# Performance work log

Hardware: AMD Instinct MI355X
Metric: run time of the kernel (lower is better)

Reference implementation:

```python
import jax, jax.numpy as jnp
import numpy as np

N_FFT = 1024
HOP = 512


def _overlap_add_50pct(frames):
    """Stateful 50% overlap-add. frames: (B, N, n_fft) -> (B, N, hop).
    Each frame is split into (curr, next); output[t] = curr[t] + next[t-1]."""
    xs = jnp.moveaxis(frames, 1, 0)  # (N, B, n_fft) for scan over frames

    def step(carry, x):
        x_curr = x[..., :HOP]
        x_next = x[..., HOP:]
        return x_next, x_curr + carry

    init = jnp.zeros((xs.shape[1], HOP), dtype=frames.dtype)
    _, ys = jax.lax.scan(step, init, xs)  # ys: (N, B, hop)
    return jnp.moveaxis(ys, 0, 1)  # (B, N, hop)


def _istft(re, im):
    spec = jax.lax.complex(re, im)               # (B, N, n_fft//2+1)
    frames = jnp.fft.irfft(spec, n=N_FFT, axis=-1)  # (B, N, n_fft), real IFFT
    frames = frames * jnp.asarray(0.5, frames.dtype)  # MulHalf (window_fn=None path)
    return _overlap_add_50pct(frames)            # (B, N, hop)


def setup_inputs() -> dict:
    key = jax.random.key(0)
    k1, k2 = jax.random.split(key)
    B, N = 8, 4000
    re = jax.random.normal(k1, (B, N, N_FFT // 2 + 1), dtype=jnp.float32)
    im = jax.random.normal(k2, (B, N, N_FFT // 2 + 1), dtype=jnp.float32)
    return {"re": re, "im": im}


def reference(re, im):
    return _istft(re, im)
```

## Files before the change

### kernel.cpp

```cpp
#include <hip/hip_runtime.h>
#include <math.h>

#define NBINS 513
#define NROWS 4000
#define BATCH 8
#define FPW   8
#define CHAINS_PER_BATCH (NROWS / FPW)

typedef const __attribute__((address_space(1))) void* gvp;
typedef __attribute__((address_space(3))) void* lvp;

__device__ __forceinline__ void cmul(float& ar, float& ai, float br, float bi) {
    const float t = ar * br - ai * bi;
    ai = ar * bi + ai * br;
    ar = t;
}

__device__ __forceinline__ void idft8(float* xr, float* xi) {
    const float S = 0.70710678118654752440f;
    float er[4], ei[4], orr[4], oi[4];
    #pragma unroll
    for (int j = 0; j < 4; ++j) {
        er[j]  = xr[j] + xr[j+4];  ei[j] = xi[j] + xi[j+4];
        orr[j] = xr[j] - xr[j+4];  oi[j] = xi[j] - xi[j+4];
    }
    const float f1r = S * (orr[1] - oi[1]), f1i = S * (orr[1] + oi[1]);
    const float f2r = -oi[2],               f2i = orr[2];
    const float f3r = S * (-orr[3] - oi[3]), f3i = S * (orr[3] - oi[3]);
    {
        const float eer = er[0]+er[2], eei = ei[0]+ei[2];
        const float eor = er[0]-er[2], eoi = ei[0]-ei[2];
        const float oer = er[1]+er[3], oei = ei[1]+ei[3];
        const float oor = er[1]-er[3], ooi = ei[1]-ei[3];
        xr[0] = eer + oer;  xi[0] = eei + oei;
        xr[2] = eor - ooi;  xi[2] = eoi + oor;
        xr[4] = eer - oer;  xi[4] = eei - oei;
        xr[6] = eor + ooi;  xi[6] = eoi - oor;
    }
    {
        const float eer = orr[0]+f2r, eei = oi[0]+f2i;
        const float eor = orr[0]-f2r, eoi = oi[0]-f2i;
        const float oer = f1r+f3r,    oei = f1i+f3i;
        const float oor = f1r-f3r,    ooi = f1i-f3i;
        xr[1] = eer + oer;  xi[1] = eei + oei;
        xr[3] = eor - ooi;  xi[3] = eoi + oor;
        xr[5] = eer - oer;  xi[5] = eei - oei;
        xr[7] = eor + ooi;  xi[7] = eoi - oor;
    }
}

__global__ __launch_bounds__(64) void istft_kernel(
    const float* __restrict__ re, const float* __restrict__ im,
    float* __restrict__ out)
{
    __shared__ float  st[2][2][516];
    __shared__ float2 ex2[512];

    const int u  = threadIdx.x;
    const int b  = blockIdx.y;
    const int t0 = blockIdx.x * FPW;

    const int k1 = u >> 3;
    const int k2 = u & 7;

    const float w0 = 6.283185307179586476925f / 1024.0f;
    const float F  = 4.8828125e-4f;

    float2 twn[8];
    #pragma unroll
    for (int j = 0; j < 8; ++j) {
        float s, c; sincosf(w0 * (float)(u + 64 * j), &s, &c);
        twn[j] = make_float2(-F * s, F * c);
    }
    float2 wA, wB0, wBs;
    {
        float s, c;
        sincosf(w0 * (float)(16 * k1), &s, &c);     wA  = make_float2(c, s);
        sincosf(w0 * (float)(2 * k2 * k1), &s, &c); wB0 = make_float2(c, s);
        sincosf(w0 * (float)(16 * k2), &s, &c);     wBs = make_float2(c, s);
    }

    float2 cc[4];
    #pragma unroll
    for (int m = 0; m < 4; ++m) cc[m] = make_float2(0.f, 0.f);

    const float* rebase = re + (size_t)b * NROWS * NBINS;
    const float* imbase = im + (size_t)b * NROWS * NBINS;

    auto stage = [&](int t, int buf) {
        const float* rp = rebase + (size_t)t * NBINS;
        const float* ip = imbase + (size_t)t * NBINS;
        #pragma unroll
        for (int jj = 0; jj < 8; ++jj)
            __builtin_amdgcn_global_load_lds((gvp)(rp + 64 * jj + u),
                                             (lvp)&st[buf][0][64 * jj], 4, 0, 0);
        __builtin_amdgcn_global_load_lds((gvp)(rp + 449 + u),
                                         (lvp)&st[buf][0][449], 4, 0, 0);
        #pragma unroll
        for (int jj = 0; jj < 8; ++jj)
            __builtin_amdgcn_global_load_lds((gvp)(ip + 64 * jj + u),
                                             (lvp)&st[buf][1][64 * jj], 4, 0, 0);
        __builtin_amdgcn_global_load_lds((gvp)(ip + 449 + u),
                                         (lvp)&st[buf][1][449], 4, 0, 0);
    };

    if (t0 == 0) {
        #pragma unroll
        for (int j = 0; j < 8; ++j) { st[0][0][u + 64 * j] = 0.f; st[0][1][u + 64 * j] = 0.f; }
        if (u == 0) { st[0][0][512] = 0.f; st[0][1][512] = 0.f; }
    } else {
        stage(t0 - 1, 0);
    }
    asm volatile("s_waitcnt vmcnt(0)" ::: "memory");

    for (int it = 0; it <= FPW; ++it) {
        const int t = t0 - 1 + it;
        const int c = it & 1;

        if (it >= 2)      { asm volatile("s_waitcnt vmcnt(8)" ::: "memory"); }
        else if (it == 1) { asm volatile("s_waitcnt vmcnt(0)" ::: "memory"); }

        float zr8[8], zi8[8];
        {
            const float* fr = st[c][0];
            const float* fi = st[c][1];
            #pragma unroll
            for (int j = 0; j < 8; ++j) {
                const int k = u + 64 * j;
                float xr = fr[k], xi = fi[k];
                float rc = fr[512 - k], ic = -fi[512 - k];
                if (k == 0) { xi = 0.f; ic = 0.f; }
                const float er0 = xr + rc, ei0 = xi + ic;
                const float hr0 = xr - rc, hi0 = xi - ic;
                zr8[j] = F * er0 + (twn[j].x * hr0 - twn[j].y * hi0);
                zi8[j] = F * ei0 + (twn[j].x * hi0 + twn[j].y * hr0);
            }
        }

        if (it < FPW) stage(t + 1, c ^ 1);

        idft8(zr8, zi8);
        {
            float tr = wA.x, ti = wA.y;
            #pragma unroll
            for (int m0 = 1; m0 < 8; ++m0) {
                cmul(zr8[m0], zi8[m0], tr, ti);
                cmul(tr, ti, wA.x, wA.y);
            }
        }
        #pragma unroll
        for (int m0 = 0; m0 < 8; ++m0)
            ex2[64 * m0 + 8 * ((k1 ^ m0) & 7) + k2] = make_float2(zr8[m0], zi8[m0]);
        #pragma unroll
        for (int kk = 0; kk < 8; ++kk) {
            const float2 v = ex2[64 * k1 + 8 * ((kk ^ k1) & 7) + k2];
            zr8[kk] = v.x; zi8[kk] = v.y;
        }

        idft8(zr8, zi8);
        {
            float tr = wB0.x, ti = wB0.y;
            #pragma unroll
            for (int m1 = 0; m1 < 8; ++m1) {
                cmul(zr8[m1], zi8[m1], tr, ti);
                cmul(tr, ti, wBs.x, wBs.y);
            }
        }
        #pragma unroll
        for (int m1 = 0; m1 < 8; ++m1)
            ex2[64 * k2 + 8 * ((m1 ^ k2) & 7) + k1] = make_float2(zr8[m1], zi8[m1]);
        #pragma unroll
        for (int kk = 0; kk < 8; ++kk) {
            const float2 v = ex2[64 * kk + 8 * ((k1 ^ kk) & 7) + k2];
            zr8[kk] = v.x; zi8[kk] = v.y;
        }

        idft8(zr8, zi8);

        if (it >= 1) {
            float2* orow = (float2*)(out + ((size_t)b * NROWS + (size_t)t) * 512);
            #pragma unroll
            for (int m = 0; m < 4; ++m)
                orow[u + 64 * m] = make_float2(zr8[m] + cc[m].x, zi8[m] + cc[m].y);
        }
        #pragma unroll
        for (int m = 0; m < 4; ++m) cc[m] = make_float2(zr8[m + 4], zi8[m + 4]);
    }
}

extern "C" void kernel_launch(void* const* d_in, const int* in_sizes, int n_in,
                              void* d_out, int out_size, void* d_ws, size_t ws_size,
                              hipStream_t stream) {
    const float* re = (const float*)d_in[0];
    const float* im = (const float*)d_in[1];
    float* out = (float*)d_out;
    dim3 grid(CHAINS_PER_BATCH, BATCH);
    istft_kernel<<<grid, 64, 0, stream>>>(re, im, out);
}
```

Before: 43.76 us.

## Replace LDS transposes in 512-point FFT with register butterfly exchanges

The two LDS exchange stages between the radix-8 passes are replaced by in-register cross-lane butterflies built from DPP, ds_swizzle and permlane16/32 swap, with a new lane permutation (su) for the twiddles and output indices. This removes the ex2 shared buffer and its store/load round trips, which also cuts LDS footprint. The wait count on the prefetch is changed to vmcnt(4). The risk is that per-element select and move overhead may cost more than the LDS traffic it replaces, and correctness depends on the lane-permutation indexing being right.

Result: slower. 47.51 us (+8.6%).

```diff
diff --git a/kernel.cpp b/kernel.cpp
--- a/kernel.cpp
+++ b/kernel.cpp
@@ -49,19 +49,65 @@
     }
 }
 
+#define BFLY_DPP(P, Q, SEL, CTRL) do {                                          \
+    float t_ = (SEL) ? (P) : (Q);                                               \
+    t_ = __int_as_float(__builtin_amdgcn_mov_dpp(__float_as_int(t_), (CTRL),    \
+                                                 0xf, 0xf, true));              \
+    (P) = (SEL) ? t_ : (P);                                                     \
+    (Q) = (SEL) ? (Q) : t_;                                                     \
+} while (0)
+
+#define BFLY_SWZ(P, Q, SEL, PAT) do {                                           \
+    float t_ = (SEL) ? (P) : (Q);                                               \
+    t_ = __int_as_float(__builtin_amdgcn_ds_swizzle(__float_as_int(t_), (PAT)));\
+    (P) = (SEL) ? t_ : (P);                                                     \
+    (Q) = (SEL) ? (Q) : t_;                                                     \
+} while (0)
+
+#if __has_builtin(__builtin_amdgcn_permlane16_swap)
+#define BFLY_PL16(P, Q, SEL) do {                                               \
+    auto r_ = __builtin_amdgcn_permlane16_swap(                                 \
+        (unsigned)__float_as_uint(P), (unsigned)__float_as_uint(Q),             \
+        false, false);                                                          \
+    (P) = __uint_as_float(r_[0]); (Q) = __uint_as_float(r_[1]);                 \
+} while (0)
+#else
+#define BFLY_PL16(P, Q, SEL) do {                                               \
+    float t_ = (SEL) ? (P) : (Q);                                               \
+    t_ = __shfl_xor(t_, 16, 64);                                                \
+    (P) = (SEL) ? t_ : (P);                                                     \
+    (Q) = (SEL) ? (Q) : t_;                                                     \
+} while (0)
+#endif
+
+#if __has_builtin(__builtin_amdgcn_permlane32_swap)
+#define BFLY_PL32(P, Q, SEL) do {                                               \
+    auto r_ = __builtin_amdgcn_permlane32_swap(                                 \
+        (unsigned)__float_as_uint(P), (unsigned)__float_as_uint(Q),             \
+        false, false);                                                          \
+    (P) = __uint_as_float(r_[0]); (Q) = __uint_as_float(r_[1]);                 \
+} while (0)
+#else
+#define BFLY_PL32(P, Q, SEL) do {                                               \
+    float t_ = (SEL) ? (P) : (Q);                                               \
+    t_ = __shfl_xor(t_, 32, 64);                                                \
+    (P) = (SEL) ? t_ : (P);                                                     \
+    (Q) = (SEL) ? (Q) : t_;                                                     \
+} while (0)
+#endif
+
 __global__ __launch_bounds__(64) void istft_kernel(
     const float* __restrict__ re, const float* __restrict__ im,
     float* __restrict__ out)
 {
-    __shared__ float  st[2][2][516];
-    __shared__ float2 ex2[512];
+    __shared__ float st[2][2][516];
 
     const int u  = threadIdx.x;
     const int b  = blockIdx.y;
     const int t0 = blockIdx.x * FPW;
 
     const int k1 = u >> 3;
-    const int k2 = u & 7;
+    const int su = ((u & 7) << 3) | k1;
 
     const float w0 = 6.283185307179586476925f / 1024.0f;
     const float F  = 4.8828125e-4f;
@@ -72,12 +118,11 @@
         float s, c; sincosf(w0 * (float)(u + 64 * j), &s, &c);
         twn[j] = make_float2(-F * s, F * c);
     }
-    float2 wA, wB0, wBs;
+    float2 wA, wB;
     {
         float s, c;
-        sincosf(w0 * (float)(16 * k1), &s, &c);     wA  = make_float2(c, s);
-        sincosf(w0 * (float)(2 * k2 * k1), &s, &c); wB0 = make_float2(c, s);
-        sincosf(w0 * (float)(16 * k2), &s, &c);     wBs = make_float2(c, s);
+        sincosf(w0 * (float)(16 * k1), &s, &c); wA = make_float2(c, s);
+        sincosf(w0 * (float)(2 * su), &s, &c);  wB = make_float2(c, s);
     }
 
     float2 cc[4];
@@ -113,11 +158,18 @@
     }
     asm volatile("s_waitcnt vmcnt(0)" ::: "memory");
 
+    const bool s1  = (u & 1)  != 0;
+    const bool s2  = (u & 2)  != 0;
+    const bool s4  = (u & 4)  != 0;
+    const bool s8  = (u & 8)  != 0;
+    const bool s16 = (u & 16) != 0; (void)s16;
+    const bool s32 = (u & 32) != 0; (void)s32;
+
     for (int it = 0; it <= FPW; ++it) {
         const int t = t0 - 1 + it;
         const int c = it & 1;
 
-        if (it >= 2)      { asm volatile("s_waitcnt vmcnt(8)" ::: "memory"); }
+        if (it >= 2)      { asm volatile("s_waitcnt vmcnt(4)" ::: "memory"); }
         else if (it == 1) { asm volatile("s_waitcnt vmcnt(0)" ::: "memory"); }
 
         float zr8[8], zi8[8];
@@ -140,48 +192,58 @@
         if (it < FPW) stage(t + 1, c ^ 1);
 
         idft8(zr8, zi8);
+
+        BFLY_DPP(zr8[0], zr8[1], s8, 0x128); BFLY_DPP(zi8[0], zi8[1], s8, 0x128);
+        BFLY_DPP(zr8[2], zr8[3], s8, 0x128); BFLY_DPP(zi8[2], zi8[3], s8, 0x128);
+        BFLY_DPP(zr8[4], zr8[5], s8, 0x128); BFLY_DPP(zi8[4], zi8[5], s8, 0x128);
+        BFLY_DPP(zr8[6], zr8[7], s8, 0x128); BFLY_DPP(zi8[6], zi8[7], s8, 0x128);
+        BFLY_PL16(zr8[0], zr8[2], s16); BFLY_PL16(zi8[0], zi8[2], s16);
+        BFLY_PL16(zr8[1], zr8[3], s16); BFLY_PL16(zi8[1], zi8[3], s16);
+        BFLY_PL16(zr8[4], zr8[6], s16); BFLY_PL16(zi8[4], zi8[6], s16);
+        BFLY_PL16(zr8[5], zr8[7], s16); BFLY_PL16(zi8[5], zi8[7], s16);
+        BFLY_PL32(zr8[0], zr8[4], s32); BFLY_PL32(zi8[0], zi8[4], s32);
+        BFLY_PL32(zr8[1], zr8[5], s32); BFLY_PL32(zi8[1], zi8[5], s32);
+        BFLY_PL32(zr8[2], zr8[6], s32); BFLY_PL32(zi8[2], zi8[6], s32);
+        BFLY_PL32(zr8[3], zr8[7], s32); BFLY_PL32(zi8[3], zi8[7], s32);
+
         {
             float tr = wA.x, ti = wA.y;
             #pragma unroll
-            for (int m0 = 1; m0 < 8; ++m0) {
-                cmul(zr8[m0], zi8[m0], tr, ti);
+            for (int r = 1; r < 8; ++r) {
+                cmul(zr8[r], zi8[r], tr, ti);
                 cmul(tr, ti, wA.x, wA.y);
             }
         }
-        #pragma unroll
-        for (int m0 = 0; m0 < 8; ++m0)
-            ex2[64 * m0 + 8 * ((k1 ^ m0) & 7) + k2] = make_float2(zr8[m0], zi8[m0]);
-        #pragma unroll
-        for (int kk = 0; kk < 8; ++kk) {
-            const float2 v = ex2[64 * k1 + 8 * ((kk ^ k1) & 7) + k2];
-            zr8[kk] = v.x; zi8[kk] = v.y;
-        }
-
         idft8(zr8, zi8);
+
+        BFLY_DPP(zr8[0], zr8[1], s1, 0xB1); BFLY_DPP(zi8[0], zi8[1], s1, 0xB1);
+        BFLY_DPP(zr8[2], zr8[3], s1, 0xB1); BFLY_DPP(zi8[2], zi8[3], s1, 0xB1);
+        BFLY_DPP(zr8[4], zr8[5], s1, 0xB1); BFLY_DPP(zi8[4], zi8[5], s1, 0xB1);
+        BFLY_DPP(zr8[6], zr8[7], s1, 0xB1); BFLY_DPP(zi8[6], zi8[7], s1, 0xB1);
+        BFLY_DPP(zr8[0], zr8[2], s2, 0x4E); BFLY_DPP(zi8[0], zi8[2], s2, 0x4E);
+        BFLY_DPP(zr8[1], zr8[3], s2, 0x4E); BFLY_DPP(zi8[1], zi8[3], s2, 0x4E);
+        BFLY_DPP(zr8[4], zr8[6], s2, 0x4E); BFLY_DPP(zi8[4], zi8[6], s2, 0x4E);
+        BFLY_DPP(zr8[5], zr8[7], s2, 0x4E); BFLY_DPP(zi8[5], zi8[7], s2, 0x4E);
+        BFLY_SWZ(zr8[0], zr8[4], s4, 0x101F); BFLY_SWZ(zi8[0], zi8[4], s4, 0x101F);
+        BFLY_SWZ(zr8[1], zr8[5], s4, 0x101F); BFLY_SWZ(zi8[1], zi8[5], s4, 0x101F);
+        BFLY_SWZ(zr8[2], zr8[6], s4, 0x101F); BFLY_SWZ(zi8[2], zi8[6], s4, 0x101F);
+        BFLY_SWZ(zr8[3], zr8[7], s4, 0x101F); BFLY_SWZ(zi8[3], zi8[7], s4, 0x101F);
+
         {
-            float tr = wB0.x, ti = wB0.y;
-            #pragma unroll
-            for (int m1 = 0; m1 < 8; ++m1) {
-                cmul(zr8[m1], zi8[m1], tr, ti);
-                cmul(tr, ti, wBs.x, wBs.y);
+            float tr = wB.x, ti = wB.y;
+            #pragma unroll
+            for (int r = 1; r < 8; ++r) {
+                cmul(zr8[r], zi8[r], tr, ti);
+                cmul(tr, ti, wB.x, wB.y);
             }
         }
-        #pragma unroll
-        for (int m1 = 0; m1 < 8; ++m1)
-            ex2[64 * k2 + 8 * ((m1 ^ k2) & 7) + k1] = make_float2(zr8[m1], zi8[m1]);
-        #pragma unroll
-        for (int kk = 0; kk < 8; ++kk) {
-            const float2 v = ex2[64 * kk + 8 * ((k1 ^ kk) & 7) + k2];
-            zr8[kk] = v.x; zi8[kk] = v.y;
-        }
-
         idft8(zr8, zi8);
 
         if (it >= 1) {
             float2* orow = (float2*)(out + ((size_t)b * NROWS + (size_t)t) * 512);
             #pragma unroll
             for (int m = 0; m < 4; ++m)
-                orow[u + 64 * m] = make_float2(zr8[m] + cc[m].x, zi8[m] + cc[m].y);
+                orow[su + 64 * m] = make_float2(zr8[m] + cc[m].x, zi8[m] + cc[m].y);
         }
         #pragma unroll
         for (int m = 0; m < 4; ++m) cc[m] = make_float2(zr8[m + 4], zi8[m + 4]);
```

## Fold overlap-add into spectrum and interleave two frames per iteration

Applied to the files above, without the earlier changes.

Each output row is now produced by a single inverse FFT of X_t + (-1)^k X_{t-1}. A 512-sample shift in a 1024-point transform is a (-1)^k phase, so this replaces the running time-domain carry and the extra leading frame per block. Two frames are processed per loop iteration, with their FFT stages and LDS transposes interleaved to add instruction-level parallelism. The LDS staging ring is widened to five buffers so two frames can be prefetched ahead. The cost is more LDS use, extra FMAs when packing spectra, and higher register pressure from holding two frames live.

Result: slower. 50.60 us (+15.6%).

```diff
diff --git a/kernel.cpp b/kernel.cpp
--- a/kernel.cpp
+++ b/kernel.cpp
@@ -5,6 +5,7 @@
 #define NROWS 4000
 #define BATCH 8
 #define FPW   8
+#define ITERS 4
 #define CHAINS_PER_BATCH (NROWS / FPW)
 
 typedef const __attribute__((address_space(1))) void* gvp;
@@ -53,7 +54,7 @@
     const float* __restrict__ re, const float* __restrict__ im,
     float* __restrict__ out)
 {
-    __shared__ float  st[2][2][516];
+    __shared__ float  st[5][2][516];
     __shared__ float2 ex2[512];
 
     const int u  = threadIdx.x;
@@ -79,10 +80,7 @@
         sincosf(w0 * (float)(2 * k2 * k1), &s, &c); wB0 = make_float2(c, s);
         sincosf(w0 * (float)(16 * k2), &s, &c);     wBs = make_float2(c, s);
     }
-
-    float2 cc[4];
-    #pragma unroll
-    for (int m = 0; m < 4; ++m) cc[m] = make_float2(0.f, 0.f);
+    const float sg = (u & 1) ? -1.0f : 1.0f;
 
     const float* rebase = re + (size_t)b * NROWS * NBINS;
     const float* imbase = im + (size_t)b * NROWS * NBINS;
@@ -104,87 +102,116 @@
                                          (lvp)&st[buf][1][449], 4, 0, 0);
     };
 
-    if (t0 == 0) {
-        #pragma unroll
-        for (int j = 0; j < 8; ++j) { st[0][0][u + 64 * j] = 0.f; st[0][1][u + 64 * j] = 0.f; }
-        if (u == 0) { st[0][0][512] = 0.f; st[0][1][512] = 0.f; }
-    } else {
-        stage(t0 - 1, 0);
-    }
-    asm volatile("s_waitcnt vmcnt(0)" ::: "memory");
-
-    for (int it = 0; it <= FPW; ++it) {
-        const int t = t0 - 1 + it;
-        const int c = it & 1;
-
-        if (it >= 2)      { asm volatile("s_waitcnt vmcnt(8)" ::: "memory"); }
-        else if (it == 1) { asm volatile("s_waitcnt vmcnt(0)" ::: "memory"); }
-
-        float zr8[8], zi8[8];
-        {
-            const float* fr = st[c][0];
-            const float* fi = st[c][1];
-            #pragma unroll
-            for (int j = 0; j < 8; ++j) {
-                const int k = u + 64 * j;
-                float xr = fr[k], xi = fi[k];
-                float rc = fr[512 - k], ic = -fi[512 - k];
-                if (k == 0) { xi = 0.f; ic = 0.f; }
-                const float er0 = xr + rc, ei0 = xi + ic;
-                const float hr0 = xr - rc, hi0 = xi - ic;
-                zr8[j] = F * er0 + (twn[j].x * hr0 - twn[j].y * hi0);
-                zi8[j] = F * ei0 + (twn[j].x * hi0 + twn[j].y * hr0);
-            }
-        }
-
-        if (it < FPW) stage(t + 1, c ^ 1);
-
+    auto pack = [&](int bp, int bc, float* zr8, float* zi8) {
+        const float* frp = st[bp][0]; const float* fip = st[bp][1];
+        const float* frc = st[bc][0]; const float* fic = st[bc][1];
+        #pragma unroll
+        for (int j = 0; j < 8; ++j) {
+            const int k = u + 64 * j;
+            float xr = fmaf(sg, frp[k], frc[k]);
+            float xi = fmaf(sg, fip[k], fic[k]);
+            float rc = fmaf(sg, frp[512 - k], frc[512 - k]);
+            float ic = -fmaf(sg, fip[512 - k], fic[512 - k]);
+            if (k == 0) { xi = 0.f; ic = 0.f; }
+            const float er0 = xr + rc, ei0 = xi + ic;
+            const float hr0 = xr - rc, hi0 = xi - ic;
+            zr8[j] = F * er0 + (twn[j].x * hr0 - twn[j].y * hi0);
+            zi8[j] = F * ei0 + (twn[j].x * hi0 + twn[j].y * hr0);
+        }
+    };
+
+    auto fftS1 = [&](float* zr8, float* zi8) {
         idft8(zr8, zi8);
-        {
-            float tr = wA.x, ti = wA.y;
-            #pragma unroll
-            for (int m0 = 1; m0 < 8; ++m0) {
-                cmul(zr8[m0], zi8[m0], tr, ti);
-                cmul(tr, ti, wA.x, wA.y);
-            }
-        }
+        float tr = wA.x, ti = wA.y;
+        #pragma unroll
+        for (int m0 = 1; m0 < 8; ++m0) {
+            cmul(zr8[m0], zi8[m0], tr, ti);
+            cmul(tr, ti, wA.x, wA.y);
+        }
+    };
+    auto x1w = [&](float* zr8, float* zi8) {
         #pragma unroll
         for (int m0 = 0; m0 < 8; ++m0)
             ex2[64 * m0 + 8 * ((k1 ^ m0) & 7) + k2] = make_float2(zr8[m0], zi8[m0]);
+    };
+    auto x1r = [&](float* zr8, float* zi8) {
         #pragma unroll
         for (int kk = 0; kk < 8; ++kk) {
             const float2 v = ex2[64 * k1 + 8 * ((kk ^ k1) & 7) + k2];
             zr8[kk] = v.x; zi8[kk] = v.y;
         }
-
+    };
+    auto fftS2 = [&](float* zr8, float* zi8) {
         idft8(zr8, zi8);
-        {
-            float tr = wB0.x, ti = wB0.y;
-            #pragma unroll
-            for (int m1 = 0; m1 < 8; ++m1) {
-                cmul(zr8[m1], zi8[m1], tr, ti);
-                cmul(tr, ti, wBs.x, wBs.y);
-            }
-        }
+        float tr = wB0.x, ti = wB0.y;
+        #pragma unroll
+        for (int m1 = 0; m1 < 8; ++m1) {
+            cmul(zr8[m1], zi8[m1], tr, ti);
+            cmul(tr, ti, wBs.x, wBs.y);
+        }
+    };
+    auto x2w = [&](float* zr8, float* zi8) {
         #pragma unroll
         for (int m1 = 0; m1 < 8; ++m1)
             ex2[64 * k2 + 8 * ((m1 ^ k2) & 7) + k1] = make_float2(zr8[m1], zi8[m1]);
+    };
+    auto x2r = [&](float* zr8, float* zi8) {
         #pragma unroll
         for (int kk = 0; kk < 8; ++kk) {
             const float2 v = ex2[64 * kk + 8 * ((k1 ^ kk) & 7) + k2];
             zr8[kk] = v.x; zi8[kk] = v.y;
         }
-
-        idft8(zr8, zi8);
-
-        if (it >= 1) {
-            float2* orow = (float2*)(out + ((size_t)b * NROWS + (size_t)t) * 512);
+    };
+
+    if (t0 == 0) {
+        #pragma unroll
+        for (int j = 0; j < 8; ++j) { st[0][0][u + 64 * j] = 0.f; st[0][1][u + 64 * j] = 0.f; }
+        if (u == 0) { st[0][0][512] = 0.f; st[0][1][512] = 0.f; }
+        stage(0, 1); stage(1, 2);
+    } else {
+        stage(t0 - 1, 0); stage(t0, 1); stage(t0 + 1, 2);
+    }
+    asm volatile("s_waitcnt vmcnt(0)" ::: "memory");
+
+    for (int i = 0; i < ITERS; ++i) {
+        const int tA = t0 + 2 * i, tB = tA + 1;
+        if (i) { asm volatile("s_waitcnt vmcnt(8)" ::: "memory"); }
+
+        float zAr[8], zAi[8], zBr[8], zBi[8];
+        pack((2 * i) % 5,     (2 * i + 1) % 5, zAr, zAi);
+        pack((2 * i + 1) % 5, (2 * i + 2) % 5, zBr, zBi);
+
+        if (i < ITERS - 1) {
+            stage(tA + 2, (2 * i + 3) % 5);
+            stage(tA + 3, (2 * i + 4) % 5);
+        }
+
+        fftS1(zAr, zAi);
+        x1w(zAr, zAi);
+        fftS1(zBr, zBi);
+        x1r(zAr, zAi);
+        x1w(zBr, zBi);
+        fftS2(zAr, zAi);
+        x1r(zBr, zBi);
+        x2w(zAr, zAi);
+        fftS2(zBr, zBi);
+        x2r(zAr, zAi);
+        x2w(zBr, zBi);
+        idft8(zAr, zAi);
+        x2r(zBr, zBi);
+        {
+            float2* orow = (float2*)(out + ((size_t)b * NROWS + (size_t)tA) * 512);
             #pragma unroll
             for (int m = 0; m < 4; ++m)
-                orow[u + 64 * m] = make_float2(zr8[m] + cc[m].x, zi8[m] + cc[m].y);
-        }
-        #pragma unroll
-        for (int m = 0; m < 4; ++m) cc[m] = make_float2(zr8[m + 4], zi8[m + 4]);
+                orow[u + 64 * m] = make_float2(zAr[m], zAi[m]);
+        }
+        idft8(zBr, zBi);
+        {
+            float2* orow = (float2*)(out + ((size_t)b * NROWS + (size_t)tB) * 512);
+            #pragma unroll
+            for (int m = 0; m < 4; ++m)
+                orow[u + 64 * m] = make_float2(zBr[m], zBi[m]);
+        }
     }
 }
 
```
